# Optimization experiments

Hardware: AMD Instinct MI355X
Metric: run time of the kernel (lower is better)

Reference implementation:

```python
import jax, jax.numpy as jnp
import numpy as np

L, H, D, FF = 6, 12, 768, 3072  # num_layers, nhead, d_model, dim_feedforward
B, N = 4, 1024                  # batch, tokens
EPS = 1e-5                      # LayerNorm eps (torch default)


def setup_inputs() -> dict:
    key = jax.random.key(0)
    ks = jax.random.split(key, 6)
    s = 0.02
    return {
        "x": jax.random.normal(ks[0], (B, N, D), jnp.float32),
        "Wqkv": jax.random.normal(ks[1], (L, 3 * D, D), jnp.float32) * s,
        "bqkv": jnp.zeros((L, 3 * D), jnp.float32),
        "Wo": jax.random.normal(ks[2], (L, D, D), jnp.float32) * s,
        "bo": jnp.zeros((L, D), jnp.float32),
        "ln1_g": jnp.ones((L, D), jnp.float32),
        "ln1_b": jnp.zeros((L, D), jnp.float32),
        "ln2_g": jnp.ones((L, D), jnp.float32),
        "ln2_b": jnp.zeros((L, D), jnp.float32),
        "W1": jax.random.normal(ks[3], (L, FF, D), jnp.float32) * s,
        "b1": jnp.zeros((L, FF), jnp.float32),
        "W2": jax.random.normal(ks[4], (L, D, FF), jnp.float32) * s,
        "b2": jnp.zeros((L, D), jnp.float32),
    }


def _ln(x, g, b):
    m = jnp.mean(x, axis=-1, keepdims=True)
    v = jnp.var(x, axis=-1, keepdims=True)
    return (x - m) * jax.lax.rsqrt(v + EPS) * g + b


def _mha(x, Wqkv, bqkv, Wo, bo):
    # nn.MultiheadAttention with need_weights=True: explicit QK^T-softmax-AV path
    b_, n_, d_ = x.shape
    dh = d_ // H
    qkv = x @ Wqkv.T + bqkv                       # [B, N, 3D]
    q, k, v = jnp.split(qkv, 3, axis=-1)
    heads = lambda t: t.reshape(b_, n_, H, dh).transpose(0, 2, 1, 3)  # [B, H, N, dh]
    q, k, v = heads(q), heads(k), heads(v)
    scores = jnp.einsum('bhnd,bhmd->bhnm', q, k) / jnp.sqrt(jnp.float32(dh))
    attn = jax.nn.softmax(scores, axis=-1)        # [B, H, N, N] (the captured weights)
    out = jnp.einsum('bhnm,bhmd->bhnd', attn, v)
    out = out.transpose(0, 2, 1, 3).reshape(b_, n_, d_)
    return out @ Wo.T + bo


def reference(x, Wqkv, bqkv, Wo, bo, ln1_g, ln1_b, ln2_g, ln2_b, W1, b1, W2, b2):
    # Faithful to the custom forward: norm1 -> MHA -> residual -> norm1 again -> FFN -> residual -> norm2
    # dropout=0.0 (eval), so dropout layers are identity.
    for l in range(L):
        src = _ln(x, ln1_g[l], ln1_b[l])
        a = _mha(src, Wqkv[l], bqkv[l], Wo[l], bo[l])
        x = _ln(x + a, ln1_g[l], ln1_b[l])
        h = jax.nn.gelu(x @ W1[l].T + b1[l], approximate=False)  # torch 'gelu' = exact erf gelu
        x = _ln(x + h @ W2[l].T + b2[l], ln2_g[l], ln2_b[l])
    return x
```

## Files before the change

### kernel.cpp

```cpp
#include <hip/hip_runtime.h>
#include <math.h>

#define DEV __device__ __forceinline__

typedef __attribute__((ext_vector_type(4))) float f32x4;
typedef __attribute__((ext_vector_type(8))) __bf16 bf16x8;
typedef __attribute__((ext_vector_type(4))) unsigned short u16x4;
typedef __attribute__((ext_vector_type(8))) unsigned short u16x8;

enum {
  LAYERS = 6, NH = 12, DM = 768, FFD = 3072, BB = 4, NT = 1024,
  MM = BB * NT,
  TD = 3 * DM
};

DEV unsigned short f2bf(float f) {
  union { float f; unsigned u; } c; c.f = f;
  unsigned u = c.u;
  return (unsigned short)((u + 0x7fffu + ((u >> 16) & 1u)) >> 16);
}

DEV void gll16(const void* gsrc, void* ldst) {
  __builtin_amdgcn_global_load_lds(
      (const __attribute__((address_space(1))) unsigned int*)gsrc,
      (__attribute__((address_space(3))) unsigned int*)ldst, 16, 0, 0);
}

DEV f32x4 mfma16(bf16x8 a, bf16x8 b, f32x4 c) {
  return __builtin_amdgcn_mfma_f32_16x16x32_bf16(a, b, c, 0, 0, 0);
}

DEV int xcd_remap(int id, int nwg) {
  const int q = nwg >> 3, r = nwg & 7;
  const int xcd = id & 7, j = id >> 3;
  return (xcd < r ? xcd * (q + 1) : r * (q + 1) + (xcd - r) * q) + j;
}

__global__ __launch_bounds__(256) void cvt4_kernel(
    const f32x4* __restrict__ i0, u16x4* __restrict__ o0, int c0,
    const f32x4* __restrict__ i1, u16x4* __restrict__ o1, int c1,
    const f32x4* __restrict__ i2, u16x4* __restrict__ o2, int c2,
    const f32x4* __restrict__ i3, u16x4* __restrict__ o3, int c3) {
  int i = blockIdx.x * 256 + threadIdx.x;
  const int stride = gridDim.x * 256;
  const int total = c0 + c1 + c2 + c3;
  for (; i < total; i += stride) {
    const f32x4* src; u16x4* dst; int k = i;
    if (k < c0) { src = i0; dst = o0; }
    else {
      k -= c0;
      if (k < c1) { src = i1; dst = o1; }
      else {
        k -= c1;
        if (k < c2) { src = i2; dst = o2; }
        else { k -= c2; src = i3; dst = o3; }
      }
    }
    f32x4 v = src[k];
    u16x4 o;
    o[0] = f2bf(v[0]); o[1] = f2bf(v[1]); o[2] = f2bf(v[2]); o[3] = f2bf(v[3]);
    dst[k] = o;
  }
}

__global__ __launch_bounds__(256) void ln_kernel(const float* __restrict__ xin,
                                                 const float* __restrict__ ain,
                                                 const float* __restrict__ ain2,
                                                 const float* __restrict__ gam,
                                                 const float* __restrict__ bet,
                                                 float* __restrict__ xout,
                                                 unsigned short* __restrict__ bfout) {
  const int row  = blockIdx.x * 4 + (threadIdx.x >> 6);
  const int lane = threadIdx.x & 63;
  const f32x4* xr = (const f32x4*)(xin + (size_t)row * DM);
  f32x4 v[3];
#pragma unroll
  for (int p = 0; p < 3; p++) v[p] = xr[lane + 64 * p];
  if (ain) {
    const f32x4* ar = (const f32x4*)(ain + (size_t)row * DM);
#pragma unroll
    for (int p = 0; p < 3; p++) v[p] += ar[lane + 64 * p];
  }
  if (ain2) {
    const f32x4* ar = (const f32x4*)(ain2 + (size_t)row * DM);
#pragma unroll
    for (int p = 0; p < 3; p++) v[p] += ar[lane + 64 * p];
  }
  float s = 0.f, sq = 0.f;
#pragma unroll
  for (int p = 0; p < 3; p++)
#pragma unroll
    for (int j = 0; j < 4; j++) { float f = v[p][j]; s += f; sq += f * f; }
#pragma unroll
  for (int o = 1; o < 64; o <<= 1) {
    s  += __shfl_xor(s, o, 64);
    sq += __shfl_xor(sq, o, 64);
  }
  const float mean = s * (1.0f / DM);
  const float var  = sq * (1.0f / DM) - mean * mean;
  const float rstd = rsqrtf(var + 1e-5f);
  const f32x4* gr = (const f32x4*)gam;
  const f32x4* br = (const f32x4*)bet;
#pragma unroll
  for (int p = 0; p < 3; p++) {
    f32x4 gv = gr[lane + 64 * p];
    f32x4 bv = br[lane + 64 * p];
    f32x4 o = (v[p] - mean) * rstd * gv + bv;
    if (xout) ((f32x4*)(xout + (size_t)row * DM))[lane + 64 * p] = o;
    if (bfout) {
      u16x4 h;
      h[0] = f2bf(o[0]); h[1] = f2bf(o[1]); h[2] = f2bf(o[2]); h[3] = f2bf(o[3]);
      ((u16x4*)(bfout + (size_t)row * DM))[lane + 64 * p] = h;
    }
  }
}

template <int EPI, int TN>
__global__ __launch_bounds__(256) void gemm_bt(const unsigned short* __restrict__ A,
                                               const unsigned short* __restrict__ Wb,
                                               const float* __restrict__ bias,
                                               void* __restrict__ Cout,
                                               int Ksz, int Nsz) {
  constexpr int BN = TN / 32;
  __shared__ alignas(16) unsigned short As[128 * 32];
  __shared__ alignas(16) unsigned short Bs[TN * 32];

  const int gx = gridDim.x, gy = gridDim.y, gz = gridDim.z;
  int id = blockIdx.x + gx * (blockIdx.y + gy * blockIdx.z);
  id = xcd_remap(id, gx * gy * gz);
  const int tz = id / (gx * gy);
  const int rem = id - tz * (gx * gy);
  const int ty = rem / gx;
  const int tx = rem - ty * gx;

  const int t = threadIdx.x;
  const int lane = t & 63;
  const int w = t >> 6;
  const int g = lane >> 4;
  const int qi = lane & 15;
  const int wr = w >> 1;
  const int wc = w & 1;
  const int m0 = ty * 128;
  const int n0 = tx * TN;
  const int ksz_per = Ksz / gz;
  const int k_begin = tz * ksz_per;
  const int k_end = k_begin + ksz_per;

  f32x4 acc[4][BN];
#pragma unroll
  for (int am = 0; am < 4; am++)
#pragma unroll
    for (int bn = 0; bn < BN; bn++) acc[am][bn] = (f32x4){0.f, 0.f, 0.f, 0.f};

  const int srow = t >> 2;
  const int schk = t & 3;
  const unsigned short* Ag = A  + (size_t)(m0 + srow) * Ksz + schk * 8;
  const unsigned short* Bg = Wb + (size_t)(n0 + srow) * Ksz + schk * 8;

  for (int kt = k_begin; kt < k_end; kt += 32) {
    __syncthreads();
    gll16(Ag + kt,                    As + srow * 32 + schk * 8);
    gll16(Ag + (size_t)64 * Ksz + kt, As + (srow + 64) * 32 + schk * 8);
    gll16(Bg + kt,                    Bs + srow * 32 + schk * 8);
    if constexpr (TN == 128)
      gll16(Bg + (size_t)64 * Ksz + kt, Bs + (srow + 64) * 32 + schk * 8);
    __syncthreads();

    bf16x8 af[4], bfr[BN];
#pragma unroll
    for (int am = 0; am < 4; am++)
      af[am] = *(const bf16x8*)(As + (wr * 64 + am * 16 + qi) * 32 + g * 8);
#pragma unroll
    for (int bn = 0; bn < BN; bn++)
      bfr[bn] = *(const bf16x8*)(Bs + (wc * (TN / 2) + bn * 16 + qi) * 32 + g * 8);
#pragma unroll
    for (int am = 0; am < 4; am++)
#pragma unroll
      for (int bn = 0; bn < BN; bn++)
        acc[am][bn] = mfma16(af[am], bfr[bn], acc[am][bn]);
  }

  float bv[BN];
#pragma unroll
  for (int bn = 0; bn < BN; bn++)
    bv[bn] = (tz == 0) ? bias[n0 + wc * (TN / 2) + bn * 16 + qi] : 0.f;

  float* Cf = (float*)Cout + (size_t)tz * ((size_t)gy * 128) * Nsz;

#pragma unroll
  for (int am = 0; am < 4; am++)
#pragma unroll
    for (int bn = 0; bn < BN; bn++)
#pragma unroll
      for (int r = 0; r < 4; r++) {
        const int mrow = m0 + wr * 64 + am * 16 + g * 4 + r;
        const int ncol = n0 + wc * (TN / 2) + bn * 16 + qi;
        float v = acc[am][bn][r] + bv[bn];
        if constexpr (EPI == 0) {
          Cf[(size_t)mrow * Nsz + ncol] = v;
        } else if constexpr (EPI == 1) {
          if (ncol < DM) v *= 0.125f;
          ((unsigned short*)Cout)[(size_t)mrow * Nsz + ncol] = f2bf(v);
        } else {
          v = 0.5f * v * (1.f + erff(v * 0.70710678118654752f));
          ((unsigned short*)Cout)[(size_t)mrow * Nsz + ncol] = f2bf(v);
        }
      }
}

__global__ __launch_bounds__(128) void attn_kernel(const unsigned short* __restrict__ qkv,
                                                   unsigned short* __restrict__ outp) {
  __shared__ alignas(16) unsigned short Ks[128 * 64];
  __shared__ alignas(16) unsigned short Vt[64 * 128];
  __shared__ alignas(16) unsigned short Ps[2][32 * 128];

  const int t = threadIdx.x;
  const int w = t >> 6;
  const int lane = t & 63;
  const int g = lane >> 4;
  const int qi = lane & 15;
  const int bidx = xcd_remap(blockIdx.x, gridDim.x);
  const int qtile = bidx & 15;
  const int bh = bidx >> 4;
  const int h = bh % NH;
  const int b = bh / NH;
  const int q0 = qtile * 64 + w * 32;
  const size_t base_bn = (size_t)b * NT;

  bf16x8 qf[2][2];
#pragma unroll
  for (int qt = 0; qt < 2; qt++)
#pragma unroll
    for (int kk = 0; kk < 2; kk++) {
      const int qrow = q0 + qt * 16 + qi;
      qf[qt][kk] = *(const bf16x8*)(qkv + (base_bn + qrow) * TD + h * 64 + kk * 32 + g * 8);
    }

  f32x4 oacc[2][4];
#pragma unroll
  for (int qt = 0; qt < 2; qt++)
#pragma unroll
    for (int dt = 0; dt < 4; dt++) oacc[qt][dt] = (f32x4){0.f, 0.f, 0.f, 0.f};
  float mval[2] = {-__builtin_inff(), -__builtin_inff()};
  float lval[2] = {0.f, 0.f};
  unsigned short* Pw = &Ps[w][0];

  for (int kv0 = 0; kv0 < NT; kv0 += 128) {
    __syncthreads();
#pragma unroll
    for (int rr = 0; rr < 8; rr++) {
      const int n = rr * 16 + (t >> 3);
      const int cd = t & 7;
      const int cg = cd ^ (n & 7);
      const unsigned short* src = qkv + (base_bn + kv0 + n) * TD + DM + h * 64 + cg * 8;
      gll16(src, Ks + n * 64 + cd * 8);
    }
#pragma unroll
    for (int r2 = 0; r2 < 2; r2++) {
      const int kb = t >> 3;
      const int d0 = r2 * 32 + (t & 7) * 4;
      u16x4 vv[8];
#pragma unroll
      for (int i = 0; i < 8; i++)
        vv[i] = *(const u16x4*)(qkv + (base_bn + kv0 + kb * 8 + i) * TD + 2 * DM + h * 64 + d0);
#pragma unroll
      for (int j = 0; j < 4; j++) {
        const int d = d0 + j;
        u16x8 w8;
#pragma unroll
        for (int i = 0; i < 8; i++) w8[i] = vv[i][j];
        *(u16x8*)((char*)Vt + d * 256 + ((kb ^ (d & 7)) * 16)) = w8;
      }
    }
    __syncthreads();

    f32x4 sacc[8][2];
#pragma unroll
    for (int nt = 0; nt < 8; nt++)
#pragma unroll
      for (int qt = 0; qt < 2; qt++) sacc[nt][qt] = (f32x4){0.f, 0.f, 0.f, 0.f};
#pragma unroll
    for (int nt = 0; nt < 8; nt++) {
      const int n = nt * 16 + qi;
      bf16x8 kf0 = *(const bf16x8*)((const char*)Ks + n * 128 + (((0 + g) ^ (n & 7)) * 16));
      bf16x8 kf1 = *(const bf16x8*)((const char*)Ks + n * 128 + (((4 + g) ^ (n & 7)) * 16));
#pragma unroll
      for (int qt = 0; qt < 2; qt++) {
        sacc[nt][qt] = mfma16(kf0, qf[qt][0], sacc[nt][qt]);
        sacc[nt][qt] = mfma16(kf1, qf[qt][1], sacc[nt][qt]);
      }
    }

#pragma unroll
    for (int qt = 0; qt < 2; qt++) {
      float mx = -__builtin_inff();
#pragma unroll
      for (int nt = 0; nt < 8; nt++)
#pragma unroll
        for (int r = 0; r < 4; r++) mx = fmaxf(mx, sacc[nt][qt][r]);
      mx = fmaxf(mx, __shfl_xor(mx, 16, 64));
      mx = fmaxf(mx, __shfl_xor(mx, 32, 64));
      const float mnew = fmaxf(mval[qt], mx);
      const float scl = __expf(mval[qt] - mnew);
      mval[qt] = mnew;
      float rsum = 0.f;
#pragma unroll
      for (int nt = 0; nt < 8; nt++)
#pragma unroll
        for (int r = 0; r < 4; r++) {
          const float p = __expf(sacc[nt][qt][r] - mnew);
          sacc[nt][qt][r] = p;
          rsum += p;
        }
      rsum += __shfl_xor(rsum, 16, 64);
      rsum += __shfl_xor(rsum, 32, 64);
      lval[qt] = lval[qt] * scl + rsum;
#pragma unroll
      for (int r = 0; r < 4; r++) {
        const float sr = __shfl(scl, g * 4 + r, 64);
#pragma unroll
        for (int dt = 0; dt < 4; dt++) oacc[qt][dt][r] *= sr;
      }
      const int qrow = qt * 16 + qi;
#pragma unroll
      for (int nt = 0; nt < 8; nt++) {
        u16x4 pk;
#pragma unroll
        for (int r = 0; r < 4; r++) pk[r] = f2bf(sacc[nt][qt][r]);
        const int byteoff = qrow * 256 + (((2 * nt + (g >> 1)) ^ (qrow & 7)) * 16) + (g & 1) * 8;
        *(u16x4*)((char*)Pw + byteoff) = pk;
      }
    }

#pragma unroll
    for (int kk2 = 0; kk2 < 4; kk2++) {
      bf16x8 pf[2], vf[4];
#pragma unroll
      for (int qt = 0; qt < 2; qt++) {
        const int qrow = qt * 16 + qi;
        pf[qt] = *(const bf16x8*)((const char*)Pw + qrow * 256 + (((kk2 * 4 + g) ^ (qrow & 7)) * 16));
      }
#pragma unroll
      for (int dt = 0; dt < 4; dt++) {
        const int d = dt * 16 + qi;
        vf[dt] = *(const bf16x8*)((const char*)Vt + d * 256 + (((kk2 * 4 + g) ^ (d & 7)) * 16));
      }
#pragma unroll
      for (int qt = 0; qt < 2; qt++)
#pragma unroll
        for (int dt = 0; dt < 4; dt++)
          oacc[qt][dt] = mfma16(pf[qt], vf[dt], oacc[qt][dt]);
    }
  }

#pragma unroll
  for (int qt = 0; qt < 2; qt++) {
    const float linv = 1.f / lval[qt];
#pragma unroll
    for (int r = 0; r < 4; r++) {
      const float lr = __shfl(linv, g * 4 + r, 64);
      const int qrow = q0 + qt * 16 + g * 4 + r;
#pragma unroll
      for (int dt = 0; dt < 4; dt++) {
        const float v = oacc[qt][dt][r] * lr;
        outp[(base_bn + qrow) * DM + h * 64 + dt * 16 + qi] = f2bf(v);
      }
    }
  }
}

extern "C" void kernel_launch(void* const* d_in, const int* in_sizes, int n_in,
                              void* d_out, int out_size, void* d_ws, size_t ws_size,
                              hipStream_t stream) {
  const float* x_in = (const float*)d_in[0];
  const float* Wqkv = (const float*)d_in[1];
  const float* bqkv = (const float*)d_in[2];
  const float* Wo   = (const float*)d_in[3];
  const float* bo   = (const float*)d_in[4];
  const float* ln1g = (const float*)d_in[5];
  const float* ln1b = (const float*)d_in[6];
  const float* ln2g = (const float*)d_in[7];
  const float* ln2b = (const float*)d_in[8];
  const float* W1   = (const float*)d_in[9];
  const float* b1   = (const float*)d_in[10];
  const float* W2   = (const float*)d_in[11];
  const float* b2   = (const float*)d_in[12];
  float* outp = (float*)d_out;

  char* ws = (char*)d_ws;
  size_t off = 0;
  auto alloc = [&](size_t bytes) {
    void* p = ws + off;
    off += (bytes + 255) & ~(size_t)255;
    return p;
  };
  unsigned short* wq_l = (unsigned short*)alloc((size_t)TD * DM * 2);
  unsigned short* wo_l = (unsigned short*)alloc((size_t)DM * DM * 2);
  unsigned short* w1_l = (unsigned short*)alloc((size_t)FFD * DM * 2);
  unsigned short* w2_l = (unsigned short*)alloc((size_t)DM * FFD * 2);
  unsigned short* src_bf  = (unsigned short*)alloc((size_t)MM * DM * 2);
  unsigned short* qkv_bf  = (unsigned short*)alloc((size_t)MM * TD * 2);
  unsigned short* attn_bf = (unsigned short*)alloc((size_t)MM * DM * 2);
  unsigned short* h_bf    = (unsigned short*)alloc((size_t)MM * FFD * 2);
  float* abuf             = (float*)alloc((size_t)2 * MM * DM * 4);
  float* x_f32            = (float*)alloc((size_t)MM * DM * 4);
  float* abuf1 = abuf + (size_t)MM * DM;

  for (int l = 0; l < LAYERS; l++) {
    const float* xcur = (l == 0) ? x_in : x_f32;
    cvt4_kernel<<<1024, 256, 0, stream>>>(
        (const f32x4*)(Wqkv + (size_t)l * TD * DM), (u16x4*)wq_l, TD * DM / 4,
        (const f32x4*)(Wo   + (size_t)l * DM * DM), (u16x4*)wo_l, DM * DM / 4,
        (const f32x4*)(W1   + (size_t)l * FFD * DM), (u16x4*)w1_l, FFD * DM / 4,
        (const f32x4*)(W2   + (size_t)l * DM * FFD), (u16x4*)w2_l, DM * FFD / 4);

    ln_kernel<<<1024, 256, 0, stream>>>(xcur, nullptr, nullptr,
                                        ln1g + l * DM, ln1b + l * DM,
                                        nullptr, src_bf);
    gemm_bt<1, 128><<<dim3(TD / 128, MM / 128), 256, 0, stream>>>(
        src_bf, wq_l, bqkv + l * TD, qkv_bf, DM, TD);
    attn_kernel<<<BB * NH * (NT / 64), 128, 0, stream>>>(qkv_bf, attn_bf);
    gemm_bt<0, 64><<<dim3(DM / 64, MM / 128, 2), 256, 0, stream>>>(
        attn_bf, wo_l, bo + l * DM, abuf, DM, DM);
    ln_kernel<<<1024, 256, 0, stream>>>(xcur, abuf, abuf1,
                                        ln1g + l * DM, ln1b + l * DM,
                                        x_f32, src_bf);
    gemm_bt<2, 128><<<dim3(FFD / 128, MM / 128), 256, 0, stream>>>(
        src_bf, w1_l, b1 + l * FFD, h_bf, DM, FFD);
    gemm_bt<0, 64><<<dim3(DM / 64, MM / 128, 2), 256, 0, stream>>>(
        h_bf, w2_l, b2 + l * DM, abuf, FFD, DM);
    ln_kernel<<<1024, 256, 0, stream>>>(x_f32, abuf, abuf1,
                                        ln2g + l * DM, ln2b + l * DM,
                                        (l == LAYERS - 1) ? outp : x_f32, nullptr);
  }
  (void)in_sizes; (void)n_in; (void)out_size; (void)ws_size;
}
```

Baseline: 1.395 ms.

## Read K directly from global in attention and defer V transpose store

After: 1.456 ms. 4.4% more time.

```diff
diff --git a/kernel.cpp b/kernel.cpp
--- a/kernel.cpp
+++ b/kernel.cpp
@@ -35,6 +35,8 @@
   const int xcd = id & 7, j = id >> 3;
   return (xcd < r ? xcd * (q + 1) : r * (q + 1) + (xcd - r) * q) + j;
 }
+
+DEV int vswz(int d) { return ((d >> 2) + 2 * (d & 3)) & 7; }
 
 __global__ __launch_bounds__(256) void cvt4_kernel(
     const f32x4* __restrict__ i0, u16x4* __restrict__ o0, int c0,
@@ -208,9 +210,8 @@
       }
 }
 
-__global__ __launch_bounds__(128) void attn_kernel(const unsigned short* __restrict__ qkv,
-                                                   unsigned short* __restrict__ outp) {
-  __shared__ alignas(16) unsigned short Ks[128 * 64];
+__global__ __launch_bounds__(128, 3) void attn_kernel(const unsigned short* __restrict__ qkv,
+                                                      unsigned short* __restrict__ outp) {
   __shared__ alignas(16) unsigned short Vt[64 * 128];
   __shared__ alignas(16) unsigned short Ps[2][32 * 128];
 
@@ -245,34 +246,21 @@
   float lval[2] = {0.f, 0.f};
   unsigned short* Pw = &Ps[w][0];
 
+  const int kb = t >> 3;
+  const unsigned short* kbase0 = qkv + base_bn * TD + DM + h * 64;
+  const unsigned short* vbase0 = qkv + base_bn * TD + 2 * DM + h * 64;
+
   for (int kv0 = 0; kv0 < NT; kv0 += 128) {
     __syncthreads();
-#pragma unroll
-    for (int rr = 0; rr < 8; rr++) {
-      const int n = rr * 16 + (t >> 3);
-      const int cd = t & 7;
-      const int cg = cd ^ (n & 7);
-      const unsigned short* src = qkv + (base_bn + kv0 + n) * TD + DM + h * 64 + cg * 8;
-      gll16(src, Ks + n * 64 + cd * 8);
-    }
+
+    u16x4 vv[2][8];
 #pragma unroll
     for (int r2 = 0; r2 < 2; r2++) {
-      const int kb = t >> 3;
       const int d0 = r2 * 32 + (t & 7) * 4;
-      u16x4 vv[8];
 #pragma unroll
       for (int i = 0; i < 8; i++)
-        vv[i] = *(const u16x4*)(qkv + (base_bn + kv0 + kb * 8 + i) * TD + 2 * DM + h * 64 + d0);
-#pragma unroll
-      for (int j = 0; j < 4; j++) {
-        const int d = d0 + j;
-        u16x8 w8;
-#pragma unroll
-        for (int i = 0; i < 8; i++) w8[i] = vv[i][j];
-        *(u16x8*)((char*)Vt + d * 256 + ((kb ^ (d & 7)) * 16)) = w8;
-      }
-    }
-    __syncthreads();
+        vv[r2][i] = *(const u16x4*)(vbase0 + (size_t)(kv0 + kb * 8 + i) * TD + d0);
+    }
 
     f32x4 sacc[8][2];
 #pragma unroll
@@ -281,9 +269,9 @@
       for (int qt = 0; qt < 2; qt++) sacc[nt][qt] = (f32x4){0.f, 0.f, 0.f, 0.f};
 #pragma unroll
     for (int nt = 0; nt < 8; nt++) {
-      const int n = nt * 16 + qi;
-      bf16x8 kf0 = *(const bf16x8*)((const char*)Ks + n * 128 + (((0 + g) ^ (n & 7)) * 16));
-      bf16x8 kf1 = *(const bf16x8*)((const char*)Ks + n * 128 + (((4 + g) ^ (n & 7)) * 16));
+      const unsigned short* kr = kbase0 + (size_t)(kv0 + nt * 16 + qi) * TD;
+      bf16x8 kf0 = *(const bf16x8*)(kr + g * 8);
+      bf16x8 kf1 = *(const bf16x8*)(kr + 32 + g * 8);
 #pragma unroll
       for (int qt = 0; qt < 2; qt++) {
         sacc[nt][qt] = mfma16(kf0, qf[qt][0], sacc[nt][qt]);
@@ -333,6 +321,20 @@
     }
 
 #pragma unroll
+    for (int r2 = 0; r2 < 2; r2++) {
+      const int d0 = r2 * 32 + (t & 7) * 4;
+#pragma unroll
+      for (int j = 0; j < 4; j++) {
+        const int d = d0 + j;
+        u16x8 w8;
+#pragma unroll
+        for (int i = 0; i < 8; i++) w8[i] = vv[r2][i][j];
+        *(u16x8*)((char*)Vt + d * 256 + ((kb ^ vswz(d)) * 16)) = w8;
+      }
+    }
+    __syncthreads();
+
+#pragma unroll
     for (int kk2 = 0; kk2 < 4; kk2++) {
       bf16x8 pf[2], vf[4];
 #pragma unroll
@@ -343,7 +345,7 @@
 #pragma unroll
       for (int dt = 0; dt < 4; dt++) {
         const int d = dt * 16 + qi;
-        vf[dt] = *(const bf16x8*)((const char*)Vt + d * 256 + (((kk2 * 4 + g) ^ (d & 7)) * 16));
+        vf[dt] = *(const bf16x8*)((const char*)Vt + d * 256 + (((kk2 * 4 + g) ^ vswz(d)) * 16));
       }
 #pragma unroll
       for (int qt = 0; qt < 2; qt++)
```
